# Performance work log

Measured on AMD Instinct MI355X. Metric: run time of the kernel, lower is better.

Reference implementation:

```python
import jax, jax.numpy as jnp
import numpy as np

H = 16        # num_attention_heads
HS = 128      # head_size
ROT = 32      # rotary_ndims (partial RoPE, NeoX rotary_pct=0.25)
BASE = 10000.0


def _rope_cache(seq_len):
    inv_freq = 1.0 / (BASE ** (jnp.arange(0, ROT, 2, dtype=jnp.float32) / ROT))
    t = jnp.arange(seq_len, dtype=jnp.float32)
    freqs = jnp.outer(t, inv_freq)                      # [s, ROT/2]
    emb = jnp.concatenate([freqs, freqs], axis=-1)      # [s, ROT]
    return jnp.cos(emb), jnp.sin(emb)


def _rotate_half(x):
    x1, x2 = jnp.split(x, 2, axis=-1)
    return jnp.concatenate([-x2, x1], axis=-1)


def setup_inputs() -> dict:
    key = jax.random.key(0)
    k1, k2, k3 = jax.random.split(key, 3)
    B, S, D = 2, 2048, 2048
    hidden_states = jax.random.normal(k1, (B, S, D), dtype=jnp.float32)
    position_ids = jnp.broadcast_to(jnp.arange(S, dtype=jnp.int64 if jax.config.jax_enable_x64 else jnp.int32), (B, S))
    W_qkv = jax.random.normal(k2, (D, 3 * H * HS), dtype=jnp.float32) * 0.02
    b_qkv = jnp.zeros((3 * H * HS,), dtype=jnp.float32)
    W_dense = jax.random.normal(k3, (H * HS, D), dtype=jnp.float32) * 0.02
    b_dense = jnp.zeros((D,), dtype=jnp.float32)
    return {"hidden_states": hidden_states, "position_ids": position_ids,
            "W_qkv": W_qkv, "b_qkv": b_qkv, "W_dense": W_dense, "b_dense": b_dense}


def reference(hidden_states, position_ids, W_qkv, b_qkv, W_dense, b_dense):
    B, S, D = hidden_states.shape
    # fused QKV projection, NeoX layout: [b, s, h, 3*hs]
    qkv = (hidden_states @ W_qkv + b_qkv).reshape(B, S, H, 3 * HS)
    q = qkv[..., :HS]            # [b, s, h, hs]
    k = qkv[..., HS:2 * HS]
    v = qkv[..., 2 * HS:]

    # partial rotary embedding on first ROT dims
    cos, sin = _rope_cache(S)                       # [s, ROT]
    cos = cos[position_ids][:, :, None, :]          # [b, s, 1, ROT]
    sin = sin[position_ids][:, :, None, :]
    q_rot, q_pass = q[..., :ROT], q[..., ROT:]
    k_rot, k_pass = k[..., :ROT], k[..., ROT:]
    q_rot = q_rot * cos + _rotate_half(q_rot) * sin
    k_rot = k_rot * cos + _rotate_half(k_rot) * sin
    q = jnp.concatenate([q_rot, q_pass], axis=-1)
    k = jnp.concatenate([k_rot, k_pass], axis=-1)

    # scaled dot-product attention (no mask, as in the source SDPA call)
    scale = 1.0 / jnp.sqrt(jnp.asarray(HS, dtype=q.dtype))
    scores = jnp.einsum('bqhd,bkhd->bhqk', q, k) * scale   # [b, h, s, s]
    attn = jax.nn.softmax(scores, axis=-1)
    out = jnp.einsum('bhqk,bkhd->bqhd', attn, v)            # [b, s, h, hs]
    out = out.reshape(B, S, H * HS)                         # 'b h d n -> b d (h n)'
    return out @ W_dense + b_dense
```

## Files before the change

kernel.cpp:

```cpp
#include <hip/hip_runtime.h>

typedef short bf16x8 __attribute__((ext_vector_type(8)));
typedef float f32x4 __attribute__((ext_vector_type(4)));

#define S_LEN 2048
#define NHEAD 16
#define HSZ 128

__device__ __forceinline__ float bf2f(ushort u) {
    union { unsigned int i; float f; } x; x.i = ((unsigned int)u) << 16; return x.f;
}
__device__ __forceinline__ ushort f2bf(float f) {
    union { float f; unsigned int i; } x; x.f = f;
    unsigned int r = (x.i + 0x7FFFu + ((x.i >> 16) & 1u)) >> 16;
    return (ushort)r;
}

__global__ void cast_kernel(const float* __restrict__ in, ushort* __restrict__ out, int n4) {
    int i = blockIdx.x * 256 + threadIdx.x;
    if (i >= n4) return;
    float4 v = ((const float4*)in)[i];
    ushort4 r;
    r.x = f2bf(v.x); r.y = f2bf(v.y); r.z = f2bf(v.z); r.w = f2bf(v.w);
    ((ushort4*)out)[i] = r;
}

__global__ void transpose_cast(const float* __restrict__ W, ushort* __restrict__ WT,
                               int K, int N) {
    __shared__ float tile[32][33];
    int n = blockIdx.x * 32 + threadIdx.x;
    #pragma unroll
    for (int j = 0; j < 32; j += 8) {
        int k = blockIdx.y * 32 + threadIdx.y + j;
        tile[threadIdx.y + j][threadIdx.x] = W[(size_t)k * N + n];
    }
    __syncthreads();
    int k2 = blockIdx.y * 32 + threadIdx.x;
    #pragma unroll
    for (int j = 0; j < 32; j += 8) {
        int n2 = blockIdx.x * 32 + threadIdx.y + j;
        WT[(size_t)n2 * K + k2] = f2bf(tile[threadIdx.x][threadIdx.y + j]);
    }
}

template <int EPI>
__global__ __launch_bounds__(256) void gemm128(
    const ushort* __restrict__ A, const ushort* __restrict__ Bt,
    const float* __restrict__ bias, float* __restrict__ Cout, int Kdim, int Ndim,
    ushort* __restrict__ q_out, ushort* __restrict__ k_out, ushort* __restrict__ v_out) {
    __shared__ __align__(16) ushort lA[128 * 32];
    __shared__ __align__(16) ushort lB[128 * 32];
    const int tid = threadIdx.x;
    const int m0 = blockIdx.y * 128, n0 = blockIdx.x * 128;
    const int lane = tid & 63, wid = tid >> 6;
    const int wm = wid >> 1, wn = wid & 1, lm = lane & 15, quad = lane >> 4;
    const int srow = tid >> 2, schunk = tid & 3;

    f32x4 acc[16];
    #pragma unroll
    for (int i = 0; i < 16; ++i) acc[i] = (f32x4){0.f, 0.f, 0.f, 0.f};

    for (int k0 = 0; k0 < Kdim; k0 += 32) {
        uint4 a0 = *(const uint4*)(A + (size_t)(m0 + srow) * Kdim + k0 + schunk * 8);
        uint4 a1 = *(const uint4*)(A + (size_t)(m0 + srow + 64) * Kdim + k0 + schunk * 8);
        uint4 b0 = *(const uint4*)(Bt + (size_t)(n0 + srow) * Kdim + k0 + schunk * 8);
        uint4 b1 = *(const uint4*)(Bt + (size_t)(n0 + srow + 64) * Kdim + k0 + schunk * 8);
        __syncthreads();
        ((uint4*)lA)[srow * 4 + schunk] = a0;
        ((uint4*)lA)[(srow + 64) * 4 + schunk] = a1;
        ((uint4*)lB)[srow * 4 + schunk] = b0;
        ((uint4*)lB)[(srow + 64) * 4 + schunk] = b1;
        __syncthreads();
        bf16x8 af[4], bfr[4];
        #pragma unroll
        for (int t = 0; t < 4; ++t) {
            af[t]  = *(const bf16x8*)(lA + (wm * 64 + t * 16 + lm) * 32 + quad * 8);
            bfr[t] = *(const bf16x8*)(lB + (wn * 64 + t * 16 + lm) * 32 + quad * 8);
        }
        #pragma unroll
        for (int mt = 0; mt < 4; ++mt)
            #pragma unroll
            for (int nt = 0; nt < 4; ++nt)
                acc[mt * 4 + nt] = __builtin_amdgcn_mfma_f32_16x16x32_bf16(
                    af[mt], bfr[nt], acc[mt * 4 + nt], 0, 0, 0);
    }

    #pragma unroll
    for (int mt = 0; mt < 4; ++mt) {
        #pragma unroll
        for (int nt = 0; nt < 4; ++nt) {
            f32x4 c = acc[mt * 4 + nt];
            int gn = n0 + wn * 64 + nt * 16 + lm;
            float bv = bias[gn];
            #pragma unroll
            for (int i = 0; i < 4; ++i) {
                int gm = m0 + wm * 64 + mt * 16 + quad * 4 + i;
                float v = c[i] + bv;
                if (EPI == 0) {
                    int h = gn / 384, r = gn - h * 384;
                    int t = r >> 7, d = r & 127;
                    int b = gm >> 11, s = gm & 2047;
                    ushort bb = f2bf(v);
                    if (t == 0) {
                        q_out[((size_t)(b * NHEAD + h) * S_LEN + s) * HSZ + d] = bb;
                    } else if (t == 1) {
                        k_out[((size_t)(b * NHEAD + h) * S_LEN + s) * HSZ + d] = bb;
                    } else {
                        v_out[((size_t)(b * NHEAD + h) * HSZ + d) * S_LEN + s] = bb;
                    }
                } else {
                    Cout[(size_t)gm * Ndim + gn] = v;
                }
            }
        }
    }
}

__global__ void rope_kernel(ushort* __restrict__ Qr, ushort* __restrict__ Kr,
                            const int* __restrict__ pos_ids) {
    int idx = blockIdx.x * 256 + threadIdx.x;
    int j = idx & 15;
    int row = idx >> 4;
    int s = row & 2047;
    int bh = row >> 11;
    int b = bh >> 4;
    int pos = pos_ids[b * S_LEN + s];
    double inv = exp2(-(double)j * (13.287712379549449 / 16.0));
    double th = (double)pos * inv;
    float c = (float)cos(th), sn = (float)sin(th);
    size_t base = (size_t)row * HSZ;
    {
        float x1 = bf2f(Qr[base + j]), x2 = bf2f(Qr[base + j + 16]);
        Qr[base + j]      = f2bf(x1 * c - x2 * sn);
        Qr[base + j + 16] = f2bf(x2 * c + x1 * sn);
    }
    {
        float x1 = bf2f(Kr[base + j]), x2 = bf2f(Kr[base + j + 16]);
        Kr[base + j]      = f2bf(x1 * c - x2 * sn);
        Kr[base + j + 16] = f2bf(x2 * c + x1 * sn);
    }
}

__global__ __launch_bounds__(256, 2) void attn_mfma(
    const ushort* __restrict__ Q, const ushort* __restrict__ K,
    const ushort* __restrict__ Vt, ushort* __restrict__ O) {
    __shared__ __align__(16) ushort lQ[128 * 136];
    __shared__ __align__(16) ushort lK[32 * 136];
    __shared__ __align__(16) ushort lVt[128 * 40];
    __shared__ __align__(16) ushort lP[4 * 32 * 40];

    const int tid = threadIdx.x;
    const int wid = tid >> 6, lane = tid & 63;
    const int L = lane & 15, quad = lane >> 4;
    const int bh = blockIdx.y;
    const int q0 = blockIdx.x * 128;
    const int wq0 = wid * 32;
    const size_t base = (size_t)bh * S_LEN * HSZ;
    const uint4* Qg = (const uint4*)(Q + base + (size_t)q0 * HSZ);
    const uint4* Kg = (const uint4*)(K + base);
    const uint4* Vg = (const uint4*)(Vt + base);
    ushort* lPw = lP + wid * (32 * 40);

    #pragma unroll
    for (int p = 0; p < 8; ++p) {
        int idx = tid + p * 256;
        int row = idx >> 4, ch = idx & 15;
        uint4 v = Qg[idx];
        *(uint4*)(lQ + row * 136 + ch * 8) = v;
    }
    __syncthreads();

    bf16x8 qf[2][4];
    #pragma unroll
    for (int qs = 0; qs < 2; ++qs)
        #pragma unroll
        for (int dc = 0; dc < 4; ++dc)
            qf[qs][dc] = *(const bf16x8*)(lQ + (wq0 + qs * 16 + L) * 136 + dc * 32 + quad * 8);

    f32x4 acc_o[8][2];
    #pragma unroll
    for (int dt = 0; dt < 8; ++dt)
        #pragma unroll
        for (int qs = 0; qs < 2; ++qs) acc_o[dt][qs] = (f32x4){0.f, 0.f, 0.f, 0.f};
    float mrow[2] = {-1e30f, -1e30f}, lrow[2] = {0.f, 0.f};
    const float scale = 0.08838834764831845f;

    for (int kt = 0; kt < S_LEN / 32; ++kt) {
        __syncthreads();
        #pragma unroll
        for (int p = 0; p < 2; ++p) {
            int idx = tid + p * 256;
            int row = idx >> 4, ch = idx & 15;
            uint4 kv = Kg[(kt * 32 + row) * 16 + ch];
            *(uint4*)(lK + row * 136 + ch * 8) = kv;
            int d = idx >> 2, c2 = idx & 3;
            uint4 vv = Vg[d * 256 + kt * 4 + c2];
            *(uint4*)(lVt + d * 40 + c2 * 8) = vv;
        }
        __syncthreads();

        f32x4 sa[2][2];
        #pragma unroll
        for (int t = 0; t < 2; ++t)
            #pragma unroll
            for (int qs = 0; qs < 2; ++qs) sa[t][qs] = (f32x4){0.f, 0.f, 0.f, 0.f};
        #pragma unroll
        for (int t = 0; t < 2; ++t)
            #pragma unroll
            for (int dc = 0; dc < 4; ++dc) {
                bf16x8 kf = *(const bf16x8*)(lK + (t * 16 + L) * 136 + dc * 32 + quad * 8);
                sa[t][0] = __builtin_amdgcn_mfma_f32_16x16x32_bf16(kf, qf[0][dc], sa[t][0], 0, 0, 0);
                sa[t][1] = __builtin_amdgcn_mfma_f32_16x16x32_bf16(kf, qf[1][dc], sa[t][1], 0, 0, 0);
            }

        float alpha[2];
        #pragma unroll
        for (int qs = 0; qs < 2; ++qs) {
            float tm = -1e30f;
            #pragma unroll
            for (int t = 0; t < 2; ++t)
                #pragma unroll
                for (int r = 0; r < 4; ++r) {
                    sa[t][qs][r] *= scale;
                    tm = fmaxf(tm, sa[t][qs][r]);
                }
            tm = fmaxf(tm, __shfl_xor(tm, 16));
            tm = fmaxf(tm, __shfl_xor(tm, 32));
            float mn = fmaxf(mrow[qs], tm);
            alpha[qs] = __expf(mrow[qs] - mn);
            float ps = 0.f;
            #pragma unroll
            for (int t = 0; t < 2; ++t)
                #pragma unroll
                for (int r = 0; r < 4; ++r) {
                    float pv = __expf(sa[t][qs][r] - mn);
                    ps += pv;
                    sa[t][qs][r] = pv;
                }
            ps += __shfl_xor(ps, 16);
            ps += __shfl_xor(ps, 32);
            lrow[qs] = lrow[qs] * alpha[qs] + ps;
            mrow[qs] = mn;
        }

        #pragma unroll
        for (int t = 0; t < 2; ++t)
            #pragma unroll
            for (int qs = 0; qs < 2; ++qs) {
                ushort4 u;
                u.x = f2bf(sa[t][qs][0]);
                u.y = f2bf(sa[t][qs][1]);
                u.z = f2bf(sa[t][qs][2]);
                u.w = f2bf(sa[t][qs][3]);
                *(ushort4*)(lPw + (qs * 16 + L) * 40 + t * 16 + quad * 4) = u;
            }
        __asm__ volatile("s_waitcnt lgkmcnt(0)" ::: "memory");

        if (__any(alpha[0] < 1.f || alpha[1] < 1.f)) {
            #pragma unroll
            for (int dt = 0; dt < 8; ++dt)
                #pragma unroll
                for (int qs = 0; qs < 2; ++qs) {
                    acc_o[dt][qs][0] *= alpha[qs];
                    acc_o[dt][qs][1] *= alpha[qs];
                    acc_o[dt][qs][2] *= alpha[qs];
                    acc_o[dt][qs][3] *= alpha[qs];
                }
        }

        bf16x8 pf0 = *(const bf16x8*)(lPw + L * 40 + quad * 8);
        bf16x8 pf1 = *(const bf16x8*)(lPw + (16 + L) * 40 + quad * 8);
        #pragma unroll
        for (int dt = 0; dt < 8; ++dt) {
            bf16x8 vf = *(const bf16x8*)(lVt + (dt * 16 + L) * 40 + quad * 8);
            acc_o[dt][0] = __builtin_amdgcn_mfma_f32_16x16x32_bf16(vf, pf0, acc_o[dt][0], 0, 0, 0);
            acc_o[dt][1] = __builtin_amdgcn_mfma_f32_16x16x32_bf16(vf, pf1, acc_o[dt][1], 0, 0, 0);
        }
    }

    const int b = bh >> 4, h = bh & 15;
    #pragma unroll
    for (int qs = 0; qs < 2; ++qs) {
        float inv = 1.f / lrow[qs];
        size_t row = ((size_t)(b * S_LEN + q0 + wq0 + qs * 16 + L)) * (NHEAD * HSZ) + h * HSZ;
        #pragma unroll
        for (int dt = 0; dt < 8; ++dt) {
            ushort4 u;
            u.x = f2bf(acc_o[dt][qs][0] * inv);
            u.y = f2bf(acc_o[dt][qs][1] * inv);
            u.z = f2bf(acc_o[dt][qs][2] * inv);
            u.w = f2bf(acc_o[dt][qs][3] * inv);
            *(ushort4*)(O + row + dt * 16 + quad * 4) = u;
        }
    }
}

extern "C" void kernel_launch(void* const* d_in, const int* in_sizes, int n_in,
                              void* d_out, int out_size, void* d_ws, size_t ws_size,
                              hipStream_t stream) {
    const float* hidden = (const float*)d_in[0];
    const int*   pos    = (const int*)d_in[1];
    const float* Wqkv   = (const float*)d_in[2];
    const float* bqkv   = (const float*)d_in[3];
    const float* Wd     = (const float*)d_in[4];
    const float* bd     = (const float*)d_in[5];

    char* ws = (char*)d_ws;
    ushort* hA  = (ushort*)ws;
    ushort* WqT = (ushort*)(ws + 16777216ull);
    ushort* WdT = (ushort*)(ws + 41943040ull);
    ushort* Qb  = (ushort*)(ws + 50331648ull);
    ushort* Kb  = (ushort*)(ws + 67108864ull);
    ushort* Vb  = (ushort*)(ws + 83886080ull);

    cast_kernel<<<dim3(8192), dim3(256), 0, stream>>>(hidden, hA, 2097152);
    transpose_cast<<<dim3(192, 64), dim3(32, 8), 0, stream>>>(Wqkv, WqT, 2048, 6144);
    transpose_cast<<<dim3(64, 64), dim3(32, 8), 0, stream>>>(Wd, WdT, 2048, 2048);

    gemm128<0><<<dim3(48, 32), dim3(256), 0, stream>>>(hA, WqT, bqkv, nullptr, 2048, 6144,
                                                       Qb, Kb, Vb);
    rope_kernel<<<dim3(4096), dim3(256), 0, stream>>>(Qb, Kb, pos);

    ushort* Obuf = hA;
    attn_mfma<<<dim3(16, 32), dim3(256), 0, stream>>>(Qb, Kb, Vb, Obuf);

    gemm128<1><<<dim3(16, 32), dim3(256), 0, stream>>>(Obuf, WdT, bd, (float*)d_out,
                                                       2048, 2048, nullptr, nullptr, nullptr);
}
```

Before: 475.5 us.

## Use direct global-to-LDS loads with XOR-swizzled shared layouts in GEMM and attention

Replaces register-staged global loads followed by LDS stores with global_load_lds 16-byte direct copies in both the GEMM and the attention K/V tile loads. Because those loads write LDS contiguously per wave, padding is removed and an XOR swizzle on the global column index plus matching read offsets is used to avoid bank conflicts. The aim is to cut VGPR traffic and instruction count on the load path. The risk is that there is still no double-buffering, so load latency stays exposed behind the barriers, and the swizzle must match exactly for correctness.

```diff
diff --git a/kernel.cpp b/kernel.cpp
--- a/kernel.cpp
+++ b/kernel.cpp
@@ -14,6 +14,13 @@
     union { float f; unsigned int i; } x; x.f = f;
     unsigned int r = (x.i + 0x7FFFu + ((x.i >> 16) & 1u)) >> 16;
     return (ushort)r;
+}
+
+__device__ __forceinline__ void gload16(const ushort* g, ushort* l) {
+    __builtin_amdgcn_global_load_lds(
+        (const __attribute__((address_space(1))) unsigned int*)g,
+        (__attribute__((address_space(3))) unsigned int*)l,
+        16, 0, 0);
 }
 
 __global__ void cast_kernel(const float* __restrict__ in, ushort* __restrict__ out, int n4) {
@@ -54,28 +61,27 @@
     const int m0 = blockIdx.y * 128, n0 = blockIdx.x * 128;
     const int lane = tid & 63, wid = tid >> 6;
     const int wm = wid >> 1, wn = wid & 1, lm = lane & 15, quad = lane >> 4;
-    const int srow = tid >> 2, schunk = tid & 3;
+    const int srow = tid >> 2;
+    const int gc = (tid & 3) ^ ((tid >> 3) & 3);
+    const int wbase = (tid >> 6) << 6;
+    const int cs = (quad ^ ((lm >> 1) & 3)) * 8;
 
     f32x4 acc[16];
     #pragma unroll
     for (int i = 0; i < 16; ++i) acc[i] = (f32x4){0.f, 0.f, 0.f, 0.f};
 
     for (int k0 = 0; k0 < Kdim; k0 += 32) {
-        uint4 a0 = *(const uint4*)(A + (size_t)(m0 + srow) * Kdim + k0 + schunk * 8);
-        uint4 a1 = *(const uint4*)(A + (size_t)(m0 + srow + 64) * Kdim + k0 + schunk * 8);
-        uint4 b0 = *(const uint4*)(Bt + (size_t)(n0 + srow) * Kdim + k0 + schunk * 8);
-        uint4 b1 = *(const uint4*)(Bt + (size_t)(n0 + srow + 64) * Kdim + k0 + schunk * 8);
         __syncthreads();
-        ((uint4*)lA)[srow * 4 + schunk] = a0;
-        ((uint4*)lA)[(srow + 64) * 4 + schunk] = a1;
-        ((uint4*)lB)[srow * 4 + schunk] = b0;
-        ((uint4*)lB)[(srow + 64) * 4 + schunk] = b1;
+        gload16(A  + (size_t)(m0 + srow)      * Kdim + k0 + gc * 8, lA + wbase * 8);
+        gload16(A  + (size_t)(m0 + srow + 64) * Kdim + k0 + gc * 8, lA + 2048 + wbase * 8);
+        gload16(Bt + (size_t)(n0 + srow)      * Kdim + k0 + gc * 8, lB + wbase * 8);
+        gload16(Bt + (size_t)(n0 + srow + 64) * Kdim + k0 + gc * 8, lB + 2048 + wbase * 8);
         __syncthreads();
         bf16x8 af[4], bfr[4];
         #pragma unroll
         for (int t = 0; t < 4; ++t) {
-            af[t]  = *(const bf16x8*)(lA + (wm * 64 + t * 16 + lm) * 32 + quad * 8);
-            bfr[t] = *(const bf16x8*)(lB + (wn * 64 + t * 16 + lm) * 32 + quad * 8);
+            af[t]  = *(const bf16x8*)(lA + (wm * 64 + t * 16 + lm) * 32 + cs);
+            bfr[t] = *(const bf16x8*)(lB + (wn * 64 + t * 16 + lm) * 32 + cs);
         }
         #pragma unroll
         for (int mt = 0; mt < 4; ++mt)
@@ -145,8 +151,8 @@
     const ushort* __restrict__ Q, const ushort* __restrict__ K,
     const ushort* __restrict__ Vt, ushort* __restrict__ O) {
     __shared__ __align__(16) ushort lQ[128 * 136];
-    __shared__ __align__(16) ushort lK[32 * 136];
-    __shared__ __align__(16) ushort lVt[128 * 40];
+    __shared__ __align__(16) ushort lK[32 * 128];
+    __shared__ __align__(16) ushort lVt[128 * 32];
     __shared__ __align__(16) ushort lP[4 * 32 * 40];
 
     const int tid = threadIdx.x;
@@ -156,16 +162,16 @@
     const int q0 = blockIdx.x * 128;
     const int wq0 = wid * 32;
     const size_t base = (size_t)bh * S_LEN * HSZ;
-    const uint4* Qg = (const uint4*)(Q + base + (size_t)q0 * HSZ);
-    const uint4* Kg = (const uint4*)(K + base);
-    const uint4* Vg = (const uint4*)(Vt + base);
+    const ushort* Qb = Q + base + (size_t)q0 * HSZ;
+    const ushort* Kb = K + base;
+    const ushort* Vb = Vt + base;
     ushort* lPw = lP + wid * (32 * 40);
 
     #pragma unroll
     for (int p = 0; p < 8; ++p) {
         int idx = tid + p * 256;
         int row = idx >> 4, ch = idx & 15;
-        uint4 v = Qg[idx];
+        uint4 v = ((const uint4*)Qb)[idx];
         *(uint4*)(lQ + row * 136 + ch * 8) = v;
     }
     __syncthreads();
@@ -176,6 +182,11 @@
         #pragma unroll
         for (int dc = 0; dc < 4; ++dc)
             qf[qs][dc] = *(const bf16x8*)(lQ + (wq0 + qs * 16 + L) * 136 + dc * 32 + quad * 8);
+
+    int kx[4];
+    #pragma unroll
+    for (int dc = 0; dc < 4; ++dc) kx[dc] = (((dc * 4 + quad) ^ (L & 7))) * 8;
+    const int vx = (quad ^ ((L >> 1) & 3)) * 8;
 
     f32x4 acc_o[8][2];
     #pragma unroll
@@ -189,13 +200,18 @@
         __syncthreads();
         #pragma unroll
         for (int p = 0; p < 2; ++p) {
-            int idx = tid + p * 256;
-            int row = idx >> 4, ch = idx & 15;
-            uint4 kv = Kg[(kt * 32 + row) * 16 + ch];
-            *(uint4*)(lK + row * 136 + ch * 8) = kv;
-            int d = idx >> 2, c2 = idx & 3;
-            uint4 vv = Vg[d * 256 + kt * 4 + c2];
-            *(uint4*)(lVt + d * 40 + c2 * 8) = vv;
+            const int li = tid + p * 256;
+            const int ub = (tid & 192) + p * 256;
+            {
+                int row = li >> 4, chp = li & 15;
+                int g = chp ^ (row & 7);
+                gload16(Kb + (size_t)(kt * 32 + row) * 128 + g * 8, lK + ub * 8);
+            }
+            {
+                int d = li >> 2, c2 = li & 3;
+                int g = c2 ^ ((d >> 1) & 3);
+                gload16(Vb + (size_t)d * 2048 + kt * 32 + g * 8, lVt + ub * 8);
+            }
         }
         __syncthreads();
 
@@ -208,7 +224,7 @@
         for (int t = 0; t < 2; ++t)
             #pragma unroll
             for (int dc = 0; dc < 4; ++dc) {
-                bf16x8 kf = *(const bf16x8*)(lK + (t * 16 + L) * 136 + dc * 32 + quad * 8);
+                bf16x8 kf = *(const bf16x8*)(lK + (t * 16 + L) * 128 + kx[dc]);
                 sa[t][0] = __builtin_amdgcn_mfma_f32_16x16x32_bf16(kf, qf[0][dc], sa[t][0], 0, 0, 0);
                 sa[t][1] = __builtin_amdgcn_mfma_f32_16x16x32_bf16(kf, qf[1][dc], sa[t][1], 0, 0, 0);
             }
@@ -272,7 +288,7 @@
         bf16x8 pf1 = *(const bf16x8*)(lPw + (16 + L) * 40 + quad * 8);
         #pragma unroll
         for (int dt = 0; dt < 8; ++dt) {
-            bf16x8 vf = *(const bf16x8*)(lVt + (dt * 16 + L) * 40 + quad * 8);
+            bf16x8 vf = *(const bf16x8*)(lVt + (dt * 16 + L) * 32 + vx);
             acc_o[dt][0] = __builtin_amdgcn_mfma_f32_16x16x32_bf16(vf, pf0, acc_o[dt][0], 0, 0, 0);
             acc_o[dt][1] = __builtin_amdgcn_mfma_f32_16x16x32_bf16(vf, pf1, acc_o[dt][1], 0, 0, 0);
         }
```

Result: no change. 477.5 us (+0.4%).
